# Kernel optimization log

Measured on AMD Instinct MI355X. Metric: run time of the kernel, lower is better.

Reference implementation:

```python
import jax, jax.numpy as jnp
import numpy as np

M, N, F = 512, 128, 512  # molecules, atoms per molecule, feature dim
HID, OUT = F // 4, 1


def setup_inputs() -> dict:
    key = jax.random.key(0)
    k1, k2, k3 = jax.random.split(key, 3)
    h = jax.random.normal(k1, (M, N, F), dtype=jnp.float32)
    W1 = jax.random.normal(k2, (F, HID), dtype=jnp.float32) * (1.0 / np.sqrt(F))
    b1 = jnp.zeros((HID,), dtype=jnp.float32)
    W2 = jax.random.normal(k3, (HID, OUT), dtype=jnp.float32) * (1.0 / np.sqrt(HID))
    b2 = jnp.zeros((OUT,), dtype=jnp.float32)
    return {"h": h, "W1": W1, "b1": b1, "W2": W2, "b2": b2}


def reference(h, W1, b1, W2, b2):
    # method == 'weighted_summation'
    # gate MLP: Linear -> ReLU -> Linear -> Sigmoid, per atom
    w = jax.nn.sigmoid(jax.nn.relu(h @ W1 + b1) @ W2 + b2)  # [M, N, OUT]
    # per-molecule weighted sum over atoms: mm(w_h.T, h) for each molecule,
    # concatenated along dim 0 -> [M*OUT, F] (OUT=1 -> [M, F])
    out = jnp.einsum('mno,mnf->mof', w, h)  # [M, OUT, F]
    return out.reshape(M * OUT, F)
```

## Files before the change

kernel.cpp:

```cpp
#include <hip/hip_runtime.h>
#include <hip/hip_bf16.h>


typedef unsigned short u16;
typedef unsigned int u32;
typedef __bf16 bf16x8 __attribute__((ext_vector_type(8)));
typedef float f32x4 __attribute__((ext_vector_type(4)));
typedef float f32x2 __attribute__((ext_vector_type(2)));
typedef u32 u32x4 __attribute__((ext_vector_type(4)));

#define M_MOL 512
#define N_ATOM 128
#define F_DIM 512
#define HID_DIM 128
#define ABLK 64
#define NBLK (M_MOL * 2)

static __device__ __forceinline__ u16 f2bf(float x) {
  u32 u = __float_as_uint(x);
  u32 r = (u + 0x7fffu + ((u >> 16) & 1u)) >> 16;
  return (u16)r;
}
static __device__ __forceinline__ bf16x8 pack8(u32x4 a, u32x4 b) {
  u32x4 r;
  r[0] = (a[0] >> 16) | (a[1] & 0xffff0000u);
  r[1] = (a[2] >> 16) | (a[3] & 0xffff0000u);
  r[2] = (b[0] >> 16) | (b[1] & 0xffff0000u);
  r[3] = (b[2] >> 16) | (b[3] & 0xffff0000u);
  return __builtin_bit_cast(bf16x8, r);
}

__global__ __launch_bounds__(256) void transpose_w1(const float* __restrict__ W1,
                                                    u16* __restrict__ W1Tt) {
  __shared__ float tile[64][65];
  const int k0 = blockIdx.x * 64;
  const int n0 = blockIdx.y * 64;
  const int t = threadIdx.x;
  #pragma unroll
  for (int i = 0; i < 16; ++i) {
    const int lin = i * 256 + t;
    const int lr = lin >> 6, lc = lin & 63;
    tile[lc][lr] = W1[(size_t)(k0 + lr) * HID_DIM + (n0 + lc)];
  }
  __syncthreads();
  #pragma unroll
  for (int i = 0; i < 16; ++i) {
    const int lin = i * 256 + t;
    const int wr = lin >> 6, wc = lin & 63;
    const int k = k0 + wc;
    W1Tt[(size_t)(k >> 5) * (HID_DIM * 32) + (size_t)(n0 + wr) * 32 + (k & 31)] =
        f2bf(tile[wr][wc]);
  }
}

__global__ __launch_bounds__(256, 2) void pool_partial(
    const float* __restrict__ h, const u16* __restrict__ W1Tt,
    const float* __restrict__ b1, const float* __restrict__ W2,
    const float* __restrict__ b2, float* __restrict__ part) {
  __shared__ u16 As[ABLK * F_DIM];
  __shared__ union U {
    u16 bt[2][HID_DIM * 32];
    struct {
      float w_s[ABLK];
      float _pad[2048 - ABLK];
      float red[4][F_DIM];
    } s;
  } sm;

  const int blk = blockIdx.x;
  const int tid = threadIdx.x;
  const int wv = tid >> 6;
  const int lane = tid & 63;
  const int quad = lane >> 4;
  const int cl = lane & 15;

  {
    const u32x4* hg = (const u32x4*)(h + (size_t)blk * ABLK * F_DIM);
    #pragma unroll
    for (int i = 0; i < 16; ++i) {
      const int u = i * 256 + tid;
      const int row = u >> 6;
      const int c = u & 63;
      u32x4 lo = hg[2 * u];
      u32x4 hi = hg[2 * u + 1];
      const int phys = (c & ~7) | ((c ^ row) & 7);
      *(bf16x8*)(As + row * F_DIM + phys * 8) = pack8(lo, hi);
    }
  }

  const u16* wg = W1Tt + tid * 16;
  const int brow = tid >> 1;
  const int bc0 = 2 * (tid & 1);
  u16* bw0 = sm.bt[0] + brow * 32;
  u16* bw1 = sm.bt[1] + brow * 32;
  const int bphysA = (bc0 ^ (brow & 3)) * 8;
  const int bphysB = ((bc0 + 1) ^ (brow & 3)) * 8;
  {
    u32x4 v0 = *(const u32x4*)wg;
    u32x4 v1 = *(const u32x4*)(wg + 8);
    *(u32x4*)(bw0 + bphysA) = v0;
    *(u32x4*)(bw0 + bphysB) = v1;
  }
  __syncthreads();

  f32x4 acc[8];
  #pragma unroll
  for (int t = 0; t < 8; ++t) acc[t] = (f32x4){0.f, 0.f, 0.f, 0.f};

  const int ar = wv * 16 + cl;
  const u16* aBase = As + ar * F_DIM;
  const int bq = (quad ^ (cl & 3)) * 8;

  for (int ks = 0; ks < 16; ++ks) {
    u32x4 v0, v1;
    if (ks < 15) {
      v0 = *(const u32x4*)(wg + (ks + 1) * (HID_DIM * 32));
      v1 = *(const u32x4*)(wg + (ks + 1) * (HID_DIM * 32) + 8);
    }
    const int c = ks * 4 + quad;
    const int aphys = (c & ~7) | ((c ^ ar) & 7);
    bf16x8 afr = *(const bf16x8*)(aBase + aphys * 8);
    const u16* btb = sm.bt[ks & 1];
    #pragma unroll
    for (int t = 0; t < 8; ++t) {
      bf16x8 bfr = *(const bf16x8*)(btb + (t * 16 + cl) * 32 + bq);
      acc[t] = __builtin_amdgcn_mfma_f32_16x16x32_bf16(afr, bfr, acc[t], 0, 0, 0);
    }
    if (ks < 15) {
      u16* bw = (ks & 1) ? bw0 : bw1;
      *(u32x4*)(bw + bphysA) = v0;
      *(u32x4*)(bw + bphysB) = v1;
      __syncthreads();
    }
  }

  float psum[4] = {0.f, 0.f, 0.f, 0.f};
  #pragma unroll
  for (int t = 0; t < 8; ++t) {
    const int hid = t * 16 + cl;
    const float b1v = b1[hid];
    const float w2v = W2[hid];
    #pragma unroll
    for (int r = 0; r < 4; ++r) {
      float tv = fmaxf(acc[t][r] + b1v, 0.f);
      psum[r] = fmaf(tv, w2v, psum[r]);
    }
  }
  #pragma unroll
  for (int off = 1; off < 16; off <<= 1)
    #pragma unroll
    for (int r = 0; r < 4; ++r)
      psum[r] += __shfl_xor(psum[r], off, 64);
  if (cl == 0) {
    const float b2v = b2[0];
    #pragma unroll
    for (int r = 0; r < 4; ++r)
      sm.s.w_s[wv * 16 + quad * 4 + r] = 1.f / (1.f + __expf(-(psum[r] + b2v)));
  }
  __syncthreads();

  float facc[8] = {0.f, 0.f, 0.f, 0.f, 0.f, 0.f, 0.f, 0.f};
  #pragma unroll 4
  for (int i = 0; i < 16; ++i) {
    const int row = wv * 16 + i;
    const float wn = sm.s.w_s[row];
    const int phys = (lane & ~7) | ((lane ^ row) & 7);
    bf16x8 hv = *(const bf16x8*)(As + row * F_DIM + phys * 8);
    u32x4 uv = __builtin_bit_cast(u32x4, hv);
    #pragma unroll
    for (int j = 0; j < 4; ++j) {
      facc[2 * j]     = fmaf(wn, __uint_as_float(uv[j] << 16), facc[2 * j]);
      facc[2 * j + 1] = fmaf(wn, __uint_as_float(uv[j] & 0xffff0000u), facc[2 * j + 1]);
    }
  }
  #pragma unroll
  for (int j = 0; j < 8; ++j) sm.s.red[wv][lane * 8 + j] = facc[j];
  __syncthreads();

  {
    const int f = tid * 2;
    f32x2 o;
    o[0] = sm.s.red[0][f] + sm.s.red[1][f] + sm.s.red[2][f] + sm.s.red[3][f];
    o[1] = sm.s.red[0][f + 1] + sm.s.red[1][f + 1] + sm.s.red[2][f + 1] + sm.s.red[3][f + 1];
    *(f32x2*)(part + (size_t)blk * F_DIM + f) = o;
  }
}

__global__ __launch_bounds__(256) void reduce_out(const float* __restrict__ part,
                                                  float* __restrict__ out) {
  const int m = blockIdx.x;
  const int f = threadIdx.x * 2;
  f32x2 a = *(const f32x2*)(part + (size_t)(2 * m) * F_DIM + f);
  f32x2 b = *(const f32x2*)(part + (size_t)(2 * m + 1) * F_DIM + f);
  f32x2 o;
  o[0] = a[0] + b[0];
  o[1] = a[1] + b[1];
  *(f32x2*)(out + (size_t)m * F_DIM + f) = o;
}

extern "C" void kernel_launch(void* const* d_in, const int* in_sizes, int n_in,
                              void* d_out, int out_size, void* d_ws, size_t ws_size,
                              hipStream_t stream) {
  const float* h  = (const float*)d_in[0];
  const float* W1 = (const float*)d_in[1];
  const float* b1 = (const float*)d_in[2];
  const float* W2 = (const float*)d_in[3];
  const float* b2 = (const float*)d_in[4];
  float* out = (float*)d_out;

  u16* W1Tt = (u16*)d_ws;
  float* part = (float*)((char*)d_ws + (size_t)HID_DIM * F_DIM * sizeof(u16));

  transpose_w1<<<dim3(8, 2), 256, 0, stream>>>(W1, W1Tt);
  pool_partial<<<NBLK, 256, 0, stream>>>(h, W1Tt, b1, W2, b2, part);
  reduce_out<<<M_MOL, 256, 0, stream>>>(part, out);
}
```

Before: 214.5 us.

## Make each wave own its rows and stream W1 fragments into registers, drop block barriers

```diff
diff --git a/kernel.cpp b/kernel.cpp
--- a/kernel.cpp
+++ b/kernel.cpp
@@ -58,14 +58,8 @@
     const float* __restrict__ b1, const float* __restrict__ W2,
     const float* __restrict__ b2, float* __restrict__ part) {
   __shared__ u16 As[ABLK * F_DIM];
-  __shared__ union U {
-    u16 bt[2][HID_DIM * 32];
-    struct {
-      float w_s[ABLK];
-      float _pad[2048 - ABLK];
-      float red[4][F_DIM];
-    } s;
-  } sm;
+  __shared__ float w_s[ABLK];
+  __shared__ float red[4][F_DIM];
 
   const int blk = blockIdx.x;
   const int tid = threadIdx.x;
@@ -74,63 +68,61 @@
   const int quad = lane >> 4;
   const int cl = lane & 15;
 
+  u16* AsW = As + wv * (16 * F_DIM);
+
   {
-    const u32x4* hg = (const u32x4*)(h + (size_t)blk * ABLK * F_DIM);
-    #pragma unroll
-    for (int i = 0; i < 16; ++i) {
-      const int u = i * 256 + tid;
-      const int row = u >> 6;
-      const int c = u & 63;
-      u32x4 lo = hg[2 * u];
-      u32x4 hi = hg[2 * u + 1];
-      const int phys = (c & ~7) | ((c ^ row) & 7);
-      *(bf16x8*)(As + row * F_DIM + phys * 8) = pack8(lo, hi);
-    }
-  }
-
-  const u16* wg = W1Tt + tid * 16;
-  const int brow = tid >> 1;
-  const int bc0 = 2 * (tid & 1);
-  u16* bw0 = sm.bt[0] + brow * 32;
-  u16* bw1 = sm.bt[1] + brow * 32;
-  const int bphysA = (bc0 ^ (brow & 3)) * 8;
-  const int bphysB = ((bc0 + 1) ^ (brow & 3)) * 8;
-  {
-    u32x4 v0 = *(const u32x4*)wg;
-    u32x4 v1 = *(const u32x4*)(wg + 8);
-    *(u32x4*)(bw0 + bphysA) = v0;
-    *(u32x4*)(bw0 + bphysB) = v1;
-  }
-  __syncthreads();
+    const float* hw = h + (size_t)blk * (ABLK * F_DIM) + (size_t)(wv * 16) * F_DIM;
+    #pragma unroll
+    for (int g = 0; g < 4; ++g) {
+      u32x4 lo[4], hi[4];
+      #pragma unroll
+      for (int i2 = 0; i2 < 4; ++i2) {
+        const int i = g * 4 + i2;
+        const u32x4* src = (const u32x4*)(hw + (size_t)i * F_DIM) + 2 * lane;
+        lo[i2] = src[0];
+        hi[i2] = src[1];
+      }
+      #pragma unroll
+      for (int i2 = 0; i2 < 4; ++i2) {
+        const int i = g * 4 + i2;
+        const int phys = (lane & ~7) | ((lane ^ i) & 7);
+        *(bf16x8*)(AsW + i * F_DIM + phys * 8) = pack8(lo[i2], hi[i2]);
+      }
+    }
+  }
+
+  const u16* bg = W1Tt + cl * 32 + quad * 8;
+  u32x4 bA[8], bB[8];
+  #pragma unroll
+  for (int t = 0; t < 8; ++t) bA[t] = *(const u32x4*)(bg + t * 512);
+
+  asm volatile("s_waitcnt lgkmcnt(0)" ::: "memory");
+  __builtin_amdgcn_sched_barrier(0);
 
   f32x4 acc[8];
   #pragma unroll
   for (int t = 0; t < 8; ++t) acc[t] = (f32x4){0.f, 0.f, 0.f, 0.f};
 
-  const int ar = wv * 16 + cl;
-  const u16* aBase = As + ar * F_DIM;
-  const int bq = (quad ^ (cl & 3)) * 8;
-
+  const u16* aBase = AsW + cl * F_DIM;
+
+  #pragma unroll
   for (int ks = 0; ks < 16; ++ks) {
-    u32x4 v0, v1;
+    const int c = ks * 4 + quad;
+    const int aphys = (c & ~7) | ((c ^ cl) & 7);
+    bf16x8 afr = *(const bf16x8*)(aBase + aphys * 8);
     if (ks < 15) {
-      v0 = *(const u32x4*)(wg + (ks + 1) * (HID_DIM * 32));
-      v1 = *(const u32x4*)(wg + (ks + 1) * (HID_DIM * 32) + 8);
-    }
-    const int c = ks * 4 + quad;
-    const int aphys = (c & ~7) | ((c ^ ar) & 7);
-    bf16x8 afr = *(const bf16x8*)(aBase + aphys * 8);
-    const u16* btb = sm.bt[ks & 1];
+      const u16* nb = bg + (size_t)(ks + 1) * (HID_DIM * 32);
+      #pragma unroll
+      for (int t = 0; t < 8; ++t) {
+        u32x4 v = *(const u32x4*)(nb + t * 512);
+        if (ks & 1) bA[t] = v; else bB[t] = v;
+      }
+    }
     #pragma unroll
     for (int t = 0; t < 8; ++t) {
-      bf16x8 bfr = *(const bf16x8*)(btb + (t * 16 + cl) * 32 + bq);
-      acc[t] = __builtin_amdgcn_mfma_f32_16x16x32_bf16(afr, bfr, acc[t], 0, 0, 0);
-    }
-    if (ks < 15) {
-      u16* bw = (ks & 1) ? bw0 : bw1;
-      *(u32x4*)(bw + bphysA) = v0;
-      *(u32x4*)(bw + bphysB) = v1;
-      __syncthreads();
+      u32x4 bv = (ks & 1) ? bB[t] : bA[t];
+      acc[t] = __builtin_amdgcn_mfma_f32_16x16x32_bf16(
+          afr, __builtin_bit_cast(bf16x8, bv), acc[t], 0, 0, 0);
     }
   }
 
@@ -155,17 +147,17 @@
     const float b2v = b2[0];
     #pragma unroll
     for (int r = 0; r < 4; ++r)
-      sm.s.w_s[wv * 16 + quad * 4 + r] = 1.f / (1.f + __expf(-(psum[r] + b2v)));
-  }
-  __syncthreads();
+      w_s[wv * 16 + quad * 4 + r] = 1.f / (1.f + __expf(-(psum[r] + b2v)));
+  }
+  asm volatile("s_waitcnt lgkmcnt(0)" ::: "memory");
+  __builtin_amdgcn_sched_barrier(0);
 
   float facc[8] = {0.f, 0.f, 0.f, 0.f, 0.f, 0.f, 0.f, 0.f};
   #pragma unroll 4
   for (int i = 0; i < 16; ++i) {
-    const int row = wv * 16 + i;
-    const float wn = sm.s.w_s[row];
-    const int phys = (lane & ~7) | ((lane ^ row) & 7);
-    bf16x8 hv = *(const bf16x8*)(As + row * F_DIM + phys * 8);
+    const float wn = w_s[wv * 16 + i];
+    const int phys = (lane & ~7) | ((lane ^ i) & 7);
+    bf16x8 hv = *(const bf16x8*)(AsW + i * F_DIM + phys * 8);
     u32x4 uv = __builtin_bit_cast(u32x4, hv);
     #pragma unroll
     for (int j = 0; j < 4; ++j) {
@@ -174,14 +166,14 @@
     }
   }
   #pragma unroll
-  for (int j = 0; j < 8; ++j) sm.s.red[wv][lane * 8 + j] = facc[j];
+  for (int j = 0; j < 8; ++j) red[wv][lane * 8 + j] = facc[j];
   __syncthreads();
 
   {
     const int f = tid * 2;
     f32x2 o;
-    o[0] = sm.s.red[0][f] + sm.s.red[1][f] + sm.s.red[2][f] + sm.s.red[3][f];
-    o[1] = sm.s.red[0][f + 1] + sm.s.red[1][f + 1] + sm.s.red[2][f + 1] + sm.s.red[3][f + 1];
+    o[0] = red[0][f] + red[1][f] + red[2][f] + red[3][f];
+    o[1] = red[0][f + 1] + red[1][f + 1] + red[2][f + 1] + red[3][f + 1];
     *(f32x2*)(part + (size_t)blk * F_DIM + f) = o;
   }
 }
```

New measurement: 215.9 us. No clear change (+0.6%).
